# Performance work log

Hardware: AMD Instinct MI355X
Metric: run time of the kernel (lower is better)

Reference implementation:

```python
import jax, jax.numpy as jnp
import numpy as np

S, B, E = 2048, 2, 1024
H = 16
HD = E // H
RANK = 8
ALPHA = 16.0
LORA_SCALE = ALPHA / RANK


def setup_inputs() -> dict:
    key = jax.random.key(0)
    ks = jax.random.split(key, 13)
    d = {
        'query': jax.random.normal(ks[0], (S, B, E), jnp.float32),
        'key': jax.random.normal(ks[1], (S, B, E), jnp.float32),
        'value': jax.random.normal(ks[2], (S, B, E), jnp.float32),
        'in_proj_weight': jax.random.normal(ks[3], (3 * E, E), jnp.float32) * 0.02,
        'in_proj_bias': jax.random.normal(ks[4], (3 * E,), jnp.float32) * 0.02,
        'out_w': jax.random.normal(ks[5], (E, E), jnp.float32) * 0.02,
        'out_b': jax.random.normal(ks[6], (E,), jnp.float32) * 0.02,
        'A_q': jax.random.normal(ks[7], (RANK, E), jnp.float32) * 0.02,
        'B_q': jax.random.normal(ks[8], (E, RANK), jnp.float32) * 0.02,
        'A_k': jax.random.normal(ks[9], (RANK, E), jnp.float32) * 0.02,
        'B_k': jax.random.normal(ks[10], (E, RANK), jnp.float32) * 0.02,
        'A_v': jax.random.normal(ks[11], (RANK, E), jnp.float32) * 0.02,
        'B_v': jax.random.normal(ks[12], (E, RANK), jnp.float32) * 0.02,
    }
    return d


def _proj(x, W, b, A, Bm):
    # frozen linear + LoRA low-rank delta: x @ W.T + b + ((x @ A.T) @ B.T) * scale
    base = jnp.einsum('sbe,fe->sbf', x, W) + b
    lora = jnp.einsum('sbr,fr->sbf', jnp.einsum('sbe,re->sbr', x, A), Bm) * LORA_SCALE
    return base + lora


def reference(query, key, value, in_proj_weight, in_proj_bias, out_w, out_b,
              A_q, B_q, A_k, B_k, A_v, B_v):
    Wq, Wk, Wv = in_proj_weight[:E], in_proj_weight[E:2 * E], in_proj_weight[2 * E:]
    bq, bk, bv = in_proj_bias[:E], in_proj_bias[E:2 * E], in_proj_bias[2 * E:]
    q = _proj(query, Wq, bq, A_q, B_q)   # [S,B,E]
    k = _proj(key, Wk, bk, A_k, B_k)
    v = _proj(value, Wv, bv, A_v, B_v)
    # reshape to [B*H, S, HD] (seq-first layout, matching torch view/transpose)
    def heads(x):
        return x.reshape(S, B * H, HD).transpose(1, 0, 2)
    qh, kh, vh = heads(q), heads(k), heads(v)
    scale = HD ** -0.5
    attn = jnp.einsum('nsd,ntd->nst', qh, kh) * scale  # [B*H,S,S]
    attn = jax.nn.softmax(attn, axis=-1)
    out = jnp.einsum('nst,ntd->nsd', attn, vh)         # [B*H,S,HD]
    out = out.transpose(1, 0, 2).reshape(S, B, E)
    out = jnp.einsum('sbe,fe->sbf', out, out_w) + out_b
    return out
```

## Files before the change

kernel.cpp:

```cpp
#include <hip/hip_runtime.h>
#include <stdint.h>

static const int S_ = 2048, B_ = 2, E_ = 1024, H_ = 16, HD_ = 64, MR_ = 4096;

typedef __bf16 bf16;
typedef __bf16 bf16x8 __attribute__((ext_vector_type(8)));
typedef float  f32x4  __attribute__((ext_vector_type(4)));
typedef float  f32x16 __attribute__((ext_vector_type(16)));
typedef unsigned short u16x8 __attribute__((ext_vector_type(8)));

#define AS1(p) ((const __attribute__((address_space(1))) void*)(p))
#define AS3(p) ((__attribute__((address_space(3))) void*)(p))

#define QSCALE 0.18033688011112042f

static __device__ __forceinline__ uint32_t cvtpk_bf16(float lo, float hi) {
    uint32_t r;
    asm("v_cvt_pk_bf16_f32 %0, %1, %2" : "=v"(r) : "v"(lo), "v"(hi));
    return r;
}

__global__ __launch_bounds__(256) void cvt_all(const float* __restrict__ s0,
                                               const float* __restrict__ s1,
                                               const float* __restrict__ s2,
                                               const float* __restrict__ s3,
                                               bf16* __restrict__ d0,
                                               bf16* __restrict__ d1,
                                               bf16* __restrict__ d2,
                                               bf16* __restrict__ d3) {
    int b = blockIdx.x;
    const float* src;
    bf16* dst;
    int i;
    if (b < 6144) {
        int seg = b >> 11;
        i = (b & 2047) * 256 + threadIdx.x;
        src = seg == 0 ? s0 : (seg == 1 ? s1 : s2);
        dst = seg == 0 ? d0 : (seg == 1 ? d1 : d2);
    } else {
        i = (b - 6144) * 256 + threadIdx.x;
        src = s3; dst = d3;
    }
    const float4* s = (const float4*)src;
    float4 a = s[i * 2], c = s[i * 2 + 1];
    bf16x8 v;
    v[0] = (bf16)a.x; v[1] = (bf16)a.y; v[2] = (bf16)a.z; v[3] = (bf16)a.w;
    v[4] = (bf16)c.x; v[5] = (bf16)c.y; v[6] = (bf16)c.z; v[7] = (bf16)c.w;
    *(bf16x8*)(dst + (size_t)i * 8) = v;
}

__global__ __launch_bounds__(256) void build_weff3(const float* __restrict__ W,
                                                   const float* __restrict__ A0,
                                                   const float* __restrict__ B0,
                                                   const float* __restrict__ A1,
                                                   const float* __restrict__ B1,
                                                   const float* __restrict__ A2,
                                                   const float* __restrict__ B2,
                                                   bf16* __restrict__ o0,
                                                   bf16* __restrict__ o1,
                                                   bf16* __restrict__ o2) {
    int z = blockIdx.y;
    const float* A = z == 0 ? A0 : (z == 1 ? A1 : A2);
    const float* Bm = z == 0 ? B0 : (z == 1 ? B1 : B2);
    bf16* out = z == 0 ? o0 : (z == 1 ? o1 : o2);
    const float* Wz = W + (size_t)z * 1024 * 1024;
    int idx = blockIdx.x * 256 + threadIdx.x;
    int f = idx >> 10, e = idx & 1023;
    float acc = Wz[idx];
#pragma unroll
    for (int r = 0; r < 8; r++) acc += 2.0f * Bm[f * 8 + r] * A[r * 1024 + e];
    out[idx] = (bf16)acc;
}

template <int MODE>
__device__ __forceinline__ void gemm_bt_body(const bf16* __restrict__ Amat,
                                             const bf16* __restrict__ Bmat,
                                             const float* __restrict__ bias,
                                             void* __restrict__ Cout, float cscale,
                                             int bx, int by) {
    __shared__ bf16 Asm[2][128 * 32];
    __shared__ bf16 Bsm[2][128 * 32];
    const int tid = threadIdx.x;
    const int wid = tid >> 6, lane = tid & 63;
    const int lg = lane >> 4, li = lane & 15;
    const int m0 = by * 128, n0 = bx * 128;
    const int wr = wid >> 1, wc = wid & 1;

    f32x4 acc[4][4] = {};

    for (int kt = 0; kt < 1024; kt += 64) {
        __syncthreads();
#pragma unroll
        for (int h = 0; h < 2; h++)
#pragma unroll
            for (int i = 0; i < 2; i++) {
                int c = wid * 2 + i;
                const bf16* ga = Amat + (size_t)(m0 + c * 16 + (lane >> 2)) * 1024 + kt + h * 32 + (lane & 3) * 8;
                __builtin_amdgcn_global_load_lds(AS1(ga), AS3(&Asm[h][c * 512]), 16, 0, 0);
                const bf16* gb = Bmat + (size_t)(n0 + c * 16 + (lane >> 2)) * 1024 + kt + h * 32 + (lane & 3) * 8;
                __builtin_amdgcn_global_load_lds(AS1(gb), AS3(&Bsm[h][c * 512]), 16, 0, 0);
            }
        __syncthreads();

#pragma unroll
        for (int h = 0; h < 2; h++) {
            bf16x8 a[4], b[4];
#pragma unroll
            for (int mi = 0; mi < 4; mi++)
                a[mi] = *(const bf16x8*)(&Asm[h][(wr * 64 + mi * 16 + li) * 32 + lg * 8]);
#pragma unroll
            for (int ni = 0; ni < 4; ni++)
                b[ni] = *(const bf16x8*)(&Bsm[h][(wc * 64 + ni * 16 + li) * 32 + lg * 8]);
#pragma unroll
            for (int mi = 0; mi < 4; mi++)
#pragma unroll
                for (int ni = 0; ni < 4; ni++)
                    acc[mi][ni] = __builtin_amdgcn_mfma_f32_16x16x32_bf16(a[mi], b[ni], acc[mi][ni], 0, 0, 0);
        }
    }

#pragma unroll
    for (int ni = 0; ni < 4; ni++) {
        int f = n0 + wc * 64 + ni * 16 + li;
        float bv = bias[f];
        if (MODE == 0) {
            bf16* out = (bf16*)Cout;
            int h = f >> 6, d = f & 63;
#pragma unroll
            for (int mi = 0; mi < 4; mi++)
#pragma unroll
                for (int r = 0; r < 4; r++) {
                    int m = m0 + wr * 64 + mi * 16 + lg * 4 + r;
                    int s = m >> 1, bb = m & 1;
                    out[(size_t)(bb * 16 + h) * S_ * 64 + (size_t)s * 64 + d] =
                        (bf16)((acc[mi][ni][r] + bv) * cscale);
                }
        } else {
            float* out = (float*)Cout;
#pragma unroll
            for (int mi = 0; mi < 4; mi++)
#pragma unroll
                for (int r = 0; r < 4; r++) {
                    int m = m0 + wr * 64 + mi * 16 + lg * 4 + r;
                    out[(size_t)m * 1024 + f] = acc[mi][ni][r] + bv;
                }
        }
    }
}

__global__ __launch_bounds__(256) void gemm_qkv(const bf16* __restrict__ XQ,
                                                const bf16* __restrict__ XK,
                                                const bf16* __restrict__ XV,
                                                const bf16* __restrict__ WQ,
                                                const bf16* __restrict__ WK,
                                                const bf16* __restrict__ WV,
                                                const float* __restrict__ ipb,
                                                bf16* __restrict__ QH,
                                                bf16* __restrict__ KH,
                                                bf16* __restrict__ VH) {
    int z = blockIdx.z;
    const bf16* A = z == 0 ? XQ : (z == 1 ? XK : XV);
    const bf16* B = z == 0 ? WQ : (z == 1 ? WK : WV);
    bf16* O = z == 0 ? QH : (z == 1 ? KH : VH);
    float sc = z == 0 ? QSCALE : 1.0f;
    gemm_bt_body<0>(A, B, ipb + z * 1024, O, sc, blockIdx.x, blockIdx.y);
}

__global__ __launch_bounds__(256) void gemm_out(const bf16* __restrict__ Amat,
                                                const bf16* __restrict__ Bmat,
                                                const float* __restrict__ bias,
                                                float* __restrict__ Cout) {
    gemm_bt_body<1>(Amat, Bmat, bias, Cout, 1.0f, blockIdx.x, blockIdx.y);
}

__global__ __launch_bounds__(256) void attn_fwd(const bf16* __restrict__ qh,
                                                const bf16* __restrict__ kh,
                                                const bf16* __restrict__ vh,
                                                bf16* __restrict__ outbuf) {
    __shared__ bf16 Ks[2][64 * 64];
    __shared__ bf16 VT[2][64 * 64];

    const int bid = blockIdx.x;
    const int head = (bid & 7) * 4 + ((bid >> 3) & 3);
    const int qt = bid >> 5;
    const int tid = threadIdx.x, wid = tid >> 6, l = tid & 63;
    const int li = l & 31, hi = l >> 5;

    const bf16* Qb = qh + (size_t)head * S_ * 64;
    const bf16* Kb = kh + (size_t)head * S_ * 64;
    const bf16* Vb = vh + (size_t)head * S_ * 64;
    const int q0 = qt * 128 + wid * 32;

    bf16x8 qf[4];
#pragma unroll
    for (int s = 0; s < 4; s++)
        qf[s] = *(const bf16x8*)(Qb + (size_t)(q0 + li) * 64 + 16 * s + 8 * hi);

    f32x16 oacc0 = {}, oacc1 = {};
    float mrun = -1e30f, lsum = 0.f;

    const int krow = tid >> 3, kc = tid & 7;
    const int kswz = 16 * (krow & 7);
    const int vk2 = tid & 31, vdb = (tid >> 5) * 8;
    const int rswz = 16 * (li & 7);

    u16x8 kreg0, kreg1, vreg0, vreg1;
    kreg0 = *(const u16x8*)(Kb + (size_t)krow * 64 + 8 * kc);
    kreg1 = *(const u16x8*)(Kb + (size_t)(krow + 32) * 64 + 8 * kc);
    vreg0 = *(const u16x8*)(Vb + (size_t)(2 * vk2) * 64 + vdb);
    vreg1 = *(const u16x8*)(Vb + (size_t)(2 * vk2 + 1) * 64 + vdb);

    for (int t = 0; t < 32; t++) {
        const int cur = t & 1;
        bf16* Kc = Ks[cur];
        bf16* Vc = VT[cur];
        *(u16x8*)((char*)Kc + krow * 128 + ((16 * kc) ^ kswz)) = kreg0;
        *(u16x8*)((char*)Kc + (krow + 32) * 128 + ((16 * kc) ^ kswz)) = kreg1;
#pragma unroll
        for (int i = 0; i < 8; i++) {
            uint32_t w = (uint32_t)vreg0[i] | ((uint32_t)vreg1[i] << 16);
            *(uint32_t*)((char*)Vc + (vdb + i) * 128 + ((4 * vk2) ^ (16 * i))) = w;
        }
        __syncthreads();
        if (t + 1 < 32) {
            int kv0 = (t + 1) * 64;
            kreg0 = *(const u16x8*)(Kb + (size_t)(kv0 + krow) * 64 + 8 * kc);
            kreg1 = *(const u16x8*)(Kb + (size_t)(kv0 + krow + 32) * 64 + 8 * kc);
            vreg0 = *(const u16x8*)(Vb + (size_t)(kv0 + 2 * vk2) * 64 + vdb);
            vreg1 = *(const u16x8*)(Vb + (size_t)(kv0 + 2 * vk2 + 1) * 64 + vdb);
        }

        f32x16 s0 = {}, s1 = {};
        __builtin_amdgcn_s_setprio(1);
#pragma unroll
        for (int step = 0; step < 4; step++) {
            bf16x8 k0 = *(const bf16x8*)((char*)Kc + li * 128 + ((32 * step + 16 * hi) ^ rswz));
            s0 = __builtin_amdgcn_mfma_f32_32x32x16_bf16(k0, qf[step], s0, 0, 0, 0);
            bf16x8 k1 = *(const bf16x8*)((char*)Kc + (32 + li) * 128 + ((32 * step + 16 * hi) ^ rswz));
            s1 = __builtin_amdgcn_mfma_f32_32x32x16_bf16(k1, qf[step], s1, 0, 0, 0);
        }
        __builtin_amdgcn_s_setprio(0);

        float lm = -1e30f;
#pragma unroll
        for (int i = 0; i < 16; i++) lm = fmaxf(lm, fmaxf(s0[i], s1[i]));
        float pmax = fmaxf(lm, __shfl_xor(lm, 32));
        bool ok = (pmax <= mrun + 8.0f);
        if (!__all(ok)) {
            float mnew = fmaxf(mrun, pmax);
            float al = __builtin_amdgcn_exp2f(mrun - mnew);
            lsum *= al;
            mrun = mnew;
#pragma unroll
            for (int r = 0; r < 16; r++) {
                float av = __shfl(al, (r & 3) + 8 * (r >> 2) + 4 * hi);
                oacc0[r] *= av;
                oacc1[r] *= av;
            }
        }

        bf16x8 pa[4];
#pragma unroll
        for (int g = 0; g < 4; g++) {
            const int rb = 8 * (g & 1);
            float p[8];
#pragma unroll
            for (int i = 0; i < 8; i++) {
                float sv = (g >> 1) ? s1[rb + i] : s0[rb + i];
                p[i] = __builtin_amdgcn_exp2f(sv - mrun);
                lsum += p[i];
            }
            uint32_t w0 = cvtpk_bf16(p[0], p[1]);
            uint32_t w1 = cvtpk_bf16(p[2], p[3]);
            uint32_t w2 = cvtpk_bf16(p[4], p[5]);
            uint32_t w3 = cvtpk_bf16(p[6], p[7]);
            uint32_t sa = hi ? w0 : w2;
            uint32_t sb = hi ? w1 : w3;
            uint32_t ea = (uint32_t)__shfl_xor((int)sa, 32);
            uint32_t eb = (uint32_t)__shfl_xor((int)sb, 32);
            union { uint32_t u[4]; bf16x8 v; } pu;
            pu.u[0] = hi ? ea : w0;
            pu.u[1] = hi ? eb : w1;
            pu.u[2] = hi ? w2 : ea;
            pu.u[3] = hi ? w3 : eb;
            pa[g] = pu.v;
        }

        __builtin_amdgcn_s_setprio(1);
#pragma unroll
        for (int g = 0; g < 4; g++) {
            bf16x8 v0 = *(const bf16x8*)((char*)Vc + li * 128 + ((32 * g + 16 * hi) ^ rswz));
            oacc0 = __builtin_amdgcn_mfma_f32_32x32x16_bf16(pa[g], v0, oacc0, 0, 0, 0);
            bf16x8 v1 = *(const bf16x8*)((char*)Vc + (32 + li) * 128 + ((32 * g + 16 * hi) ^ rswz));
            oacc1 = __builtin_amdgcn_mfma_f32_32x32x16_bf16(pa[g], v1, oacc1, 0, 0, 0);
        }
        __builtin_amdgcn_s_setprio(0);
    }

    float lt = lsum + __shfl_xor(lsum, 32);
    float linv = 1.0f / lt;
    int bb = head >> 4, h = head & 15;
#pragma unroll
    for (int r = 0; r < 16; r++) {
        int rp = (r & 3) + 8 * (r >> 2) + 4 * hi;
        float lv = __shfl(linv, rp);
        int q = q0 + rp;
        size_t row = (size_t)(q * 2 + bb) * 1024 + h * 64;
        outbuf[row + li] = (bf16)(oacc0[r] * lv);
        outbuf[row + 32 + li] = (bf16)(oacc1[r] * lv);
    }
}

extern "C" void kernel_launch(void* const* d_in, const int* in_sizes, int n_in,
                              void* d_out, int out_size, void* d_ws, size_t ws_size,
                              hipStream_t stream) {
    const float* query = (const float*)d_in[0];
    const float* key_  = (const float*)d_in[1];
    const float* value = (const float*)d_in[2];
    const float* ipw   = (const float*)d_in[3];
    const float* ipb   = (const float*)d_in[4];
    const float* out_w = (const float*)d_in[5];
    const float* out_b = (const float*)d_in[6];
    const float* A_q   = (const float*)d_in[7];
    const float* B_q   = (const float*)d_in[8];
    const float* A_k   = (const float*)d_in[9];
    const float* B_k   = (const float*)d_in[10];
    const float* A_v   = (const float*)d_in[11];
    const float* B_v   = (const float*)d_in[12];

    const size_t MB = 1ull << 20;
    if (ws_size < 64 * MB) return;
    char* ws = (char*)d_ws;
    bf16* XQ = (bf16*)(ws + 0 * MB);
    bf16* XK = (bf16*)(ws + 8 * MB);
    bf16* XV = (bf16*)(ws + 16 * MB);
    bf16* WQ = (bf16*)(ws + 24 * MB);
    bf16* WK = (bf16*)(ws + 26 * MB);
    bf16* WV = (bf16*)(ws + 28 * MB);
    bf16* WO = (bf16*)(ws + 30 * MB);
    bf16* QH = (bf16*)(ws + 32 * MB);
    bf16* KH = (bf16*)(ws + 40 * MB);
    bf16* VH = (bf16*)(ws + 48 * MB);
    bf16* AT = (bf16*)(ws + 56 * MB);

    cvt_all<<<6656, 256, 0, stream>>>(query, key_, value, out_w, XQ, XK, XV, WO);
    build_weff3<<<dim3(4096, 3), 256, 0, stream>>>(ipw, A_q, B_q, A_k, B_k, A_v, B_v,
                                                   WQ, WK, WV);

    gemm_qkv<<<dim3(8, 32, 3), 256, 0, stream>>>(XQ, XK, XV, WQ, WK, WV, ipb, QH, KH, VH);

    attn_fwd<<<512, 256, 0, stream>>>(QH, KH, VH, AT);

    gemm_out<<<dim3(8, 32), 256, 0, stream>>>(AT, WO, out_b, (float*)d_out);
}
```

Before: 152.7 us.

## Split attention KV across wave pairs and shrink output GEMM tiles

New measurement: 152.6 us. Within noise of the previous version (-0.0%).

```diff
diff --git a/kernel.cpp b/kernel.cpp
--- a/kernel.cpp
+++ b/kernel.cpp
@@ -72,82 +72,6 @@
     out[idx] = (bf16)acc;
 }
 
-template <int MODE>
-__device__ __forceinline__ void gemm_bt_body(const bf16* __restrict__ Amat,
-                                             const bf16* __restrict__ Bmat,
-                                             const float* __restrict__ bias,
-                                             void* __restrict__ Cout, float cscale,
-                                             int bx, int by) {
-    __shared__ bf16 Asm[2][128 * 32];
-    __shared__ bf16 Bsm[2][128 * 32];
-    const int tid = threadIdx.x;
-    const int wid = tid >> 6, lane = tid & 63;
-    const int lg = lane >> 4, li = lane & 15;
-    const int m0 = by * 128, n0 = bx * 128;
-    const int wr = wid >> 1, wc = wid & 1;
-
-    f32x4 acc[4][4] = {};
-
-    for (int kt = 0; kt < 1024; kt += 64) {
-        __syncthreads();
-#pragma unroll
-        for (int h = 0; h < 2; h++)
-#pragma unroll
-            for (int i = 0; i < 2; i++) {
-                int c = wid * 2 + i;
-                const bf16* ga = Amat + (size_t)(m0 + c * 16 + (lane >> 2)) * 1024 + kt + h * 32 + (lane & 3) * 8;
-                __builtin_amdgcn_global_load_lds(AS1(ga), AS3(&Asm[h][c * 512]), 16, 0, 0);
-                const bf16* gb = Bmat + (size_t)(n0 + c * 16 + (lane >> 2)) * 1024 + kt + h * 32 + (lane & 3) * 8;
-                __builtin_amdgcn_global_load_lds(AS1(gb), AS3(&Bsm[h][c * 512]), 16, 0, 0);
-            }
-        __syncthreads();
-
-#pragma unroll
-        for (int h = 0; h < 2; h++) {
-            bf16x8 a[4], b[4];
-#pragma unroll
-            for (int mi = 0; mi < 4; mi++)
-                a[mi] = *(const bf16x8*)(&Asm[h][(wr * 64 + mi * 16 + li) * 32 + lg * 8]);
-#pragma unroll
-            for (int ni = 0; ni < 4; ni++)
-                b[ni] = *(const bf16x8*)(&Bsm[h][(wc * 64 + ni * 16 + li) * 32 + lg * 8]);
-#pragma unroll
-            for (int mi = 0; mi < 4; mi++)
-#pragma unroll
-                for (int ni = 0; ni < 4; ni++)
-                    acc[mi][ni] = __builtin_amdgcn_mfma_f32_16x16x32_bf16(a[mi], b[ni], acc[mi][ni], 0, 0, 0);
-        }
-    }
-
-#pragma unroll
-    for (int ni = 0; ni < 4; ni++) {
-        int f = n0 + wc * 64 + ni * 16 + li;
-        float bv = bias[f];
-        if (MODE == 0) {
-            bf16* out = (bf16*)Cout;
-            int h = f >> 6, d = f & 63;
-#pragma unroll
-            for (int mi = 0; mi < 4; mi++)
-#pragma unroll
-                for (int r = 0; r < 4; r++) {
-                    int m = m0 + wr * 64 + mi * 16 + lg * 4 + r;
-                    int s = m >> 1, bb = m & 1;
-                    out[(size_t)(bb * 16 + h) * S_ * 64 + (size_t)s * 64 + d] =
-                        (bf16)((acc[mi][ni][r] + bv) * cscale);
-                }
-        } else {
-            float* out = (float*)Cout;
-#pragma unroll
-            for (int mi = 0; mi < 4; mi++)
-#pragma unroll
-                for (int r = 0; r < 4; r++) {
-                    int m = m0 + wr * 64 + mi * 16 + lg * 4 + r;
-                    out[(size_t)m * 1024 + f] = acc[mi][ni][r] + bv;
-                }
-        }
-    }
-}
-
 __global__ __launch_bounds__(256) void gemm_qkv(const bf16* __restrict__ XQ,
                                                 const bf16* __restrict__ XK,
                                                 const bf16* __restrict__ XV,
@@ -159,37 +83,148 @@
                                                 bf16* __restrict__ KH,
                                                 bf16* __restrict__ VH) {
     int z = blockIdx.z;
-    const bf16* A = z == 0 ? XQ : (z == 1 ? XK : XV);
-    const bf16* B = z == 0 ? WQ : (z == 1 ? WK : WV);
-    bf16* O = z == 0 ? QH : (z == 1 ? KH : VH);
-    float sc = z == 0 ? QSCALE : 1.0f;
-    gemm_bt_body<0>(A, B, ipb + z * 1024, O, sc, blockIdx.x, blockIdx.y);
-}
-
-__global__ __launch_bounds__(256) void gemm_out(const bf16* __restrict__ Amat,
-                                                const bf16* __restrict__ Bmat,
-                                                const float* __restrict__ bias,
-                                                float* __restrict__ Cout) {
-    gemm_bt_body<1>(Amat, Bmat, bias, Cout, 1.0f, blockIdx.x, blockIdx.y);
-}
-
-__global__ __launch_bounds__(256) void attn_fwd(const bf16* __restrict__ qh,
-                                                const bf16* __restrict__ kh,
-                                                const bf16* __restrict__ vh,
-                                                bf16* __restrict__ outbuf) {
-    __shared__ bf16 Ks[2][64 * 64];
-    __shared__ bf16 VT[2][64 * 64];
+    const bf16* Amat = z == 0 ? XQ : (z == 1 ? XK : XV);
+    const bf16* Bmat = z == 0 ? WQ : (z == 1 ? WK : WV);
+    bf16* Cout = z == 0 ? QH : (z == 1 ? KH : VH);
+    const float* bias = ipb + z * 1024;
+    float cscale = z == 0 ? QSCALE : 1.0f;
+
+    __shared__ bf16 Asm[2][128 * 32];
+    __shared__ bf16 Bsm[2][128 * 32];
+    const int tid = threadIdx.x;
+    const int wid = tid >> 6, lane = tid & 63;
+    const int lg = lane >> 4, li = lane & 15;
+    const int m0 = blockIdx.y * 128, n0 = blockIdx.x * 128;
+    const int wr = wid >> 1, wc = wid & 1;
+
+    f32x4 acc[4][4] = {};
+
+    for (int kt = 0; kt < 1024; kt += 64) {
+        __syncthreads();
+#pragma unroll
+        for (int h = 0; h < 2; h++)
+#pragma unroll
+            for (int i = 0; i < 2; i++) {
+                int c = wid * 2 + i;
+                const bf16* ga = Amat + (size_t)(m0 + c * 16 + (lane >> 2)) * 1024 + kt + h * 32 + (lane & 3) * 8;
+                __builtin_amdgcn_global_load_lds(AS1(ga), AS3(&Asm[h][c * 512]), 16, 0, 0);
+                const bf16* gb = Bmat + (size_t)(n0 + c * 16 + (lane >> 2)) * 1024 + kt + h * 32 + (lane & 3) * 8;
+                __builtin_amdgcn_global_load_lds(AS1(gb), AS3(&Bsm[h][c * 512]), 16, 0, 0);
+            }
+        __syncthreads();
+
+#pragma unroll
+        for (int h = 0; h < 2; h++) {
+            bf16x8 a[4], b[4];
+#pragma unroll
+            for (int mi = 0; mi < 4; mi++)
+                a[mi] = *(const bf16x8*)(&Asm[h][(wr * 64 + mi * 16 + li) * 32 + lg * 8]);
+#pragma unroll
+            for (int ni = 0; ni < 4; ni++)
+                b[ni] = *(const bf16x8*)(&Bsm[h][(wc * 64 + ni * 16 + li) * 32 + lg * 8]);
+#pragma unroll
+            for (int mi = 0; mi < 4; mi++)
+#pragma unroll
+                for (int ni = 0; ni < 4; ni++)
+                    acc[mi][ni] = __builtin_amdgcn_mfma_f32_16x16x32_bf16(a[mi], b[ni], acc[mi][ni], 0, 0, 0);
+        }
+    }
+
+#pragma unroll
+    for (int ni = 0; ni < 4; ni++) {
+        int f = n0 + wc * 64 + ni * 16 + li;
+        float bv = bias[f];
+        int h = f >> 6, d = f & 63;
+#pragma unroll
+        for (int mi = 0; mi < 4; mi++)
+#pragma unroll
+            for (int r = 0; r < 4; r++) {
+                int m = m0 + wr * 64 + mi * 16 + lg * 4 + r;
+                int s = m >> 1, bb = m & 1;
+                Cout[(size_t)(bb * 16 + h) * S_ * 64 + (size_t)s * 64 + d] =
+                    (bf16)((acc[mi][ni][r] + bv) * cscale);
+            }
+    }
+}
+
+__global__ __launch_bounds__(256) void gemm_out64(const bf16* __restrict__ Amat,
+                                                  const bf16* __restrict__ Bmat,
+                                                  const float* __restrict__ bias,
+                                                  float* __restrict__ Cout) {
+    __shared__ bf16 Asm[2][64 * 32];
+    __shared__ bf16 Bsm[2][128 * 32];
+    const int tid = threadIdx.x;
+    const int wid = tid >> 6, lane = tid & 63;
+    const int lg = lane >> 4, li = lane & 15;
+    const int m0 = blockIdx.y * 64, n0 = blockIdx.x * 128;
+    const int wr = wid >> 1, wc = wid & 1;
+
+    f32x4 acc[2][4] = {};
+
+    for (int kt = 0; kt < 1024; kt += 64) {
+        __syncthreads();
+#pragma unroll
+        for (int h = 0; h < 2; h++)
+            for (int j = wid; j < 12; j += 4) {
+                if (j < 4) {
+                    const bf16* ga = Amat + (size_t)(m0 + j * 16 + (lane >> 2)) * 1024 + kt + h * 32 + (lane & 3) * 8;
+                    __builtin_amdgcn_global_load_lds(AS1(ga), AS3(&Asm[h][j * 512]), 16, 0, 0);
+                } else {
+                    int c = j - 4;
+                    const bf16* gb = Bmat + (size_t)(n0 + c * 16 + (lane >> 2)) * 1024 + kt + h * 32 + (lane & 3) * 8;
+                    __builtin_amdgcn_global_load_lds(AS1(gb), AS3(&Bsm[h][c * 512]), 16, 0, 0);
+                }
+            }
+        __syncthreads();
+
+#pragma unroll
+        for (int h = 0; h < 2; h++) {
+            bf16x8 a[2], b[4];
+#pragma unroll
+            for (int mi = 0; mi < 2; mi++)
+                a[mi] = *(const bf16x8*)(&Asm[h][(wr * 32 + mi * 16 + li) * 32 + lg * 8]);
+#pragma unroll
+            for (int ni = 0; ni < 4; ni++)
+                b[ni] = *(const bf16x8*)(&Bsm[h][(wc * 64 + ni * 16 + li) * 32 + lg * 8]);
+#pragma unroll
+            for (int mi = 0; mi < 2; mi++)
+#pragma unroll
+                for (int ni = 0; ni < 4; ni++)
+                    acc[mi][ni] = __builtin_amdgcn_mfma_f32_16x16x32_bf16(a[mi], b[ni], acc[mi][ni], 0, 0, 0);
+        }
+    }
+
+#pragma unroll
+    for (int ni = 0; ni < 4; ni++) {
+        int f = n0 + wc * 64 + ni * 16 + li;
+        float bv = bias[f];
+#pragma unroll
+        for (int mi = 0; mi < 2; mi++)
+#pragma unroll
+            for (int r = 0; r < 4; r++) {
+                int m = m0 + wr * 32 + mi * 16 + lg * 4 + r;
+                Cout[(size_t)m * 1024 + f] = acc[mi][ni][r] + bv;
+            }
+    }
+}
+
+__global__ __launch_bounds__(256, 4) void attn_fwd(const bf16* __restrict__ qh,
+                                                   const bf16* __restrict__ kh,
+                                                   const bf16* __restrict__ vh,
+                                                   bf16* __restrict__ outbuf) {
+    __shared__ __attribute__((aligned(16))) char smem[33792];
 
     const int bid = blockIdx.x;
     const int head = (bid & 7) * 4 + ((bid >> 3) & 3);
     const int qt = bid >> 5;
     const int tid = threadIdx.x, wid = tid >> 6, l = tid & 63;
     const int li = l & 31, hi = l >> 5;
+    const int kvh = wid & 1;
 
     const bf16* Qb = qh + (size_t)head * S_ * 64;
     const bf16* Kb = kh + (size_t)head * S_ * 64;
     const bf16* Vb = vh + (size_t)head * S_ * 64;
-    const int q0 = qt * 128 + wid * 32;
+    const int q0 = qt * 64 + (wid >> 1) * 32;
 
     bf16x8 qf[4];
 #pragma unroll
@@ -212,14 +247,14 @@
 
     for (int t = 0; t < 32; t++) {
         const int cur = t & 1;
-        bf16* Kc = Ks[cur];
-        bf16* Vc = VT[cur];
-        *(u16x8*)((char*)Kc + krow * 128 + ((16 * kc) ^ kswz)) = kreg0;
-        *(u16x8*)((char*)Kc + (krow + 32) * 128 + ((16 * kc) ^ kswz)) = kreg1;
+        char* Kc = smem + cur * 8192;
+        char* Vc = smem + 16384 + cur * 8192;
+        *(u16x8*)(Kc + krow * 128 + ((16 * kc) ^ kswz)) = kreg0;
+        *(u16x8*)(Kc + (krow + 32) * 128 + ((16 * kc) ^ kswz)) = kreg1;
 #pragma unroll
         for (int i = 0; i < 8; i++) {
             uint32_t w = (uint32_t)vreg0[i] | ((uint32_t)vreg1[i] << 16);
-            *(uint32_t*)((char*)Vc + (vdb + i) * 128 + ((4 * vk2) ^ (16 * i))) = w;
+            *(uint32_t*)(Vc + (vdb + i) * 128 + ((4 * vk2) ^ (16 * i))) = w;
         }
         __syncthreads();
         if (t + 1 < 32) {
@@ -230,20 +265,18 @@
             vreg1 = *(const u16x8*)(Vb + (size_t)(kv0 + 2 * vk2 + 1) * 64 + vdb);
         }
 
-        f32x16 s0 = {}, s1 = {};
+        f32x16 s = {};
         __builtin_amdgcn_s_setprio(1);
 #pragma unroll
         for (int step = 0; step < 4; step++) {
-            bf16x8 k0 = *(const bf16x8*)((char*)Kc + li * 128 + ((32 * step + 16 * hi) ^ rswz));
-            s0 = __builtin_amdgcn_mfma_f32_32x32x16_bf16(k0, qf[step], s0, 0, 0, 0);
-            bf16x8 k1 = *(const bf16x8*)((char*)Kc + (32 + li) * 128 + ((32 * step + 16 * hi) ^ rswz));
-            s1 = __builtin_amdgcn_mfma_f32_32x32x16_bf16(k1, qf[step], s1, 0, 0, 0);
+            bf16x8 k0 = *(const bf16x8*)(Kc + (kvh * 32 + li) * 128 + ((32 * step + 16 * hi) ^ rswz));
+            s = __builtin_amdgcn_mfma_f32_32x32x16_bf16(k0, qf[step], s, 0, 0, 0);
         }
         __builtin_amdgcn_s_setprio(0);
 
         float lm = -1e30f;
 #pragma unroll
-        for (int i = 0; i < 16; i++) lm = fmaxf(lm, fmaxf(s0[i], s1[i]));
+        for (int i = 0; i < 16; i++) lm = fmaxf(lm, s[i]);
         float pmax = fmaxf(lm, __shfl_xor(lm, 32));
         bool ok = (pmax <= mrun + 8.0f);
         if (!__all(ok)) {
@@ -259,15 +292,13 @@
             }
         }
 
-        bf16x8 pa[4];
-#pragma unroll
-        for (int g = 0; g < 4; g++) {
-            const int rb = 8 * (g & 1);
+        bf16x8 pa[2];
+#pragma unroll
+        for (int g = 0; g < 2; g++) {
             float p[8];
 #pragma unroll
             for (int i = 0; i < 8; i++) {
-                float sv = (g >> 1) ? s1[rb + i] : s0[rb + i];
-                p[i] = __builtin_amdgcn_exp2f(sv - mrun);
+                p[i] = __builtin_amdgcn_exp2f(s[8 * g + i] - mrun);
                 lsum += p[i];
             }
             uint32_t w0 = cvtpk_bf16(p[0], p[1]);
@@ -288,26 +319,47 @@
 
         __builtin_amdgcn_s_setprio(1);
 #pragma unroll
-        for (int g = 0; g < 4; g++) {
-            bf16x8 v0 = *(const bf16x8*)((char*)Vc + li * 128 + ((32 * g + 16 * hi) ^ rswz));
+        for (int g = 0; g < 2; g++) {
+            int kvb = 64 * kvh + 32 * g + 16 * hi;
+            bf16x8 v0 = *(const bf16x8*)(Vc + li * 128 + (kvb ^ rswz));
             oacc0 = __builtin_amdgcn_mfma_f32_32x32x16_bf16(pa[g], v0, oacc0, 0, 0, 0);
-            bf16x8 v1 = *(const bf16x8*)((char*)Vc + (32 + li) * 128 + ((32 * g + 16 * hi) ^ rswz));
+            bf16x8 v1 = *(const bf16x8*)(Vc + (32 + li) * 128 + (kvb ^ rswz));
             oacc1 = __builtin_amdgcn_mfma_f32_32x32x16_bf16(pa[g], v1, oacc1, 0, 0, 0);
         }
         __builtin_amdgcn_s_setprio(0);
     }
 
+    __syncthreads();
+    float* ml = (float*)(smem + 32768);
+    float* scr = (float*)smem;
     float lt = lsum + __shfl_xor(lsum, 32);
-    float linv = 1.0f / lt;
+    if (l < 32) { ml[wid * 64 + l] = mrun; ml[wid * 64 + 32 + l] = lt; }
+    {
+        float* mys = scr + wid * 1024;
+#pragma unroll
+        for (int r = 0; r < 16; r++) {
+            int rp = (r & 3) + 8 * (r >> 2) + 4 * hi;
+            mys[rp * 32 + li] = kvh ? oacc0[r] : oacc1[r];
+        }
+    }
+    __syncthreads();
+    float pm = ml[(wid ^ 1) * 64 + li];
+    float pl = ml[(wid ^ 1) * 64 + 32 + li];
+    float m = fmaxf(mrun, pm);
+    float sc = __builtin_amdgcn_exp2f(mrun - m);
+    float sco = __builtin_amdgcn_exp2f(pm - m);
+    float linv = 1.0f / (lt * sc + pl * sco);
+    float a1 = sc * linv, a2 = sco * linv;
+    const float* ps = scr + (wid ^ 1) * 1024;
     int bb = head >> 4, h = head & 15;
 #pragma unroll
     for (int r = 0; r < 16; r++) {
         int rp = (r & 3) + 8 * (r >> 2) + 4 * hi;
-        float lv = __shfl(linv, rp);
         int q = q0 + rp;
-        size_t row = (size_t)(q * 2 + bb) * 1024 + h * 64;
-        outbuf[row + li] = (bf16)(oacc0[r] * lv);
-        outbuf[row + 32 + li] = (bf16)(oacc1[r] * lv);
+        float own = kvh ? oacc1[r] : oacc0[r];
+        float part = ps[rp * 32 + li];
+        float val = own * __shfl(a1, rp) + part * __shfl(a2, rp);
+        outbuf[(size_t)(q * 2 + bb) * 1024 + h * 64 + kvh * 32 + li] = (bf16)val;
     }
 }
 
@@ -349,7 +401,7 @@
 
     gemm_qkv<<<dim3(8, 32, 3), 256, 0, stream>>>(XQ, XK, XV, WQ, WK, WV, ipb, QH, KH, VH);
 
-    attn_fwd<<<512, 256, 0, stream>>>(QH, KH, VH, AT);
-
-    gemm_out<<<dim3(8, 32), 256, 0, stream>>>(AT, WO, out_b, (float*)d_out);
-}
+    attn_fwd<<<1024, 256, 0, stream>>>(QH, KH, VH, AT);
+
+    gemm_out64<<<dim3(8, 64), 256, 0, stream>>>(AT, WO, out_b, (float*)d_out);
+}
```
